# Performance work log

Hardware: AMD Instinct MI355X
Metric: run time of the kernel (lower is better)

Reference implementation:

```python
import jax, jax.numpy as jnp
import numpy as np
import math

N_B = 4
SHAPES = np.array([[100, 100], [50, 50], [25, 25], [13, 13]], dtype=np.int32)
C = 256
M = 8   # heads
L = 4   # levels
P = 4   # points
D = C // M


def _grid_init_bias():
    # matches reset_parameters: per-head directional offsets scaled by point index
    thetas = np.arange(M, dtype=np.float64) * (2.0 * math.pi / M)
    g = np.stack([np.cos(thetas), np.sin(thetas)], -1)
    g = g / np.abs(g).max(-1, keepdims=True)
    g = np.tile(g.reshape(M, 1, 1, 2), (1, L, P, 1))
    g = g * (np.arange(P, dtype=np.float64) + 1.0).reshape(1, 1, P, 1)
    return jnp.asarray(g.reshape(-1), dtype=jnp.float32)


def setup_inputs() -> dict:
    key = jax.random.key(0)
    ks = jax.random.split(key, 10)
    len_in = int((SHAPES[:, 0] * SHAPES[:, 1]).sum())  # 13294
    lq = len_in
    query = jax.random.normal(ks[0], (N_B, lq, C), dtype=jnp.float32)
    reference_points = jax.random.uniform(ks[1], (N_B, lq, L, 2), dtype=jnp.float32)
    input_flatten = jax.random.normal(ks[2], (N_B, len_in, C), dtype=jnp.float32)
    starts = np.concatenate([[0], np.cumsum(SHAPES[:, 0] * SHAPES[:, 1])[:-1]]).astype(np.int32)
    inv_sq = 1.0 / math.sqrt(C)
    Wv = jax.random.normal(ks[3], (C, C), dtype=jnp.float32) * inv_sq
    bv = jnp.zeros((C,), jnp.float32)
    Wo = jax.random.normal(ks[4], (C, C), dtype=jnp.float32) * inv_sq
    bo = jnp.zeros((C,), jnp.float32)
    # torch init zeros these weights; small random values keep the sampling
    # pattern query-dependent (more representative workload)
    W_off = jax.random.normal(ks[5], (C, M * L * P * 2), dtype=jnp.float32) * 1e-3
    b_off = _grid_init_bias()
    W_attn = jax.random.normal(ks[6], (C, M * L * P), dtype=jnp.float32) * 1e-2
    b_attn = jnp.zeros((M * L * P,), jnp.float32)
    return {
        "query": query,
        "reference_points": reference_points,
        "input_flatten": input_flatten,
        "input_space_shape": jnp.asarray(SHAPES),
        "input_level_start_idx": jnp.asarray(starts),
        "Wv": Wv, "bv": bv,
        "W_off": W_off, "b_off": b_off,
        "W_attn": W_attn, "b_attn": b_attn,
        "Wo": Wo, "bo": bo,
    }


def _bilinear_sample(v, lx, ly, H, W):
    """v: (N, M, H*W, D); lx, ly: (N, M, Lq, P) normalized coords in [0,1].
    Equivalent to F.grid_sample(mode='bilinear', padding_mode='zeros',
    align_corners=False) with grid = 2*loc - 1: pixel x = loc*W - 0.5.
    Returns (N, M, Lq, P, D)."""
    n, m, lq, p = lx.shape
    d = v.shape[-1]
    x = lx * W - 0.5
    y = ly * H - 0.5
    x0 = jnp.floor(x)
    y0 = jnp.floor(y)
    wx = x - x0
    wy = y - y0
    x0i = x0.astype(jnp.int32)
    y0i = y0.astype(jnp.int32)
    acc = jnp.zeros((n, m, lq, p, d), dtype=v.dtype)
    corners = [
        (0, 0, (1.0 - wx) * (1.0 - wy)),
        (1, 0, wx * (1.0 - wy)),
        (0, 1, (1.0 - wx) * wy),
        (1, 1, wx * wy),
    ]
    for dx, dy, w in corners:
        xi = x0i + dx
        yi = y0i + dy
        valid = ((xi >= 0) & (xi < W) & (yi >= 0) & (yi < H)).astype(v.dtype)
        idx = jnp.clip(yi, 0, H - 1) * W + jnp.clip(xi, 0, W - 1)  # (N,M,Lq,P)
        g = jnp.take_along_axis(v, idx.reshape(n, m, -1)[..., None], axis=2)
        g = g.reshape(n, m, lq, p, d)
        acc = acc + g * (w * valid)[..., None]
    return acc


def reference(query, reference_points, input_flatten, input_space_shape,
              input_level_start_idx, Wv, bv, W_off, b_off, W_attn, b_attn, Wo, bo):
    n, lq, c = query.shape
    shapes = np.asarray(input_space_shape)  # static (L, 2)
    # value projection -> (N, Len_in, M, D)
    value = (input_flatten @ Wv + bv).reshape(n, -1, M, D)
    # sampling offsets (N, Lq, M, L, P, 2)
    off = (query @ W_off + b_off).reshape(n, lq, M, L, P, 2)
    # attention weights, softmax over L*P
    aw = jax.nn.softmax((query @ W_attn + b_attn).reshape(n, lq, M, L * P), axis=-1)
    aw = aw.reshape(n, lq, M, L, P)
    # normalized sampling locations in [0,1]
    norm = jnp.stack([input_space_shape[:, 1], input_space_shape[:, 0]], -1).astype(query.dtype)  # (L,2) = (W,H)
    loc = reference_points[:, :, None, :, None, :] + off / norm[None, None, None, :, None, :]
    out = jnp.zeros((n, lq, M, D), dtype=query.dtype)
    start = 0
    for lvl in range(shapes.shape[0]):
        H_, W_ = int(shapes[lvl, 0]), int(shapes[lvl, 1])
        v = value[:, start:start + H_ * W_].transpose(0, 2, 1, 3)  # (N, M, HW, D)
        lx = loc[:, :, :, lvl, :, 0].transpose(0, 2, 1, 3)  # (N, M, Lq, P)
        ly = loc[:, :, :, lvl, :, 1].transpose(0, 2, 1, 3)
        s = _bilinear_sample(v, lx, ly, H_, W_)  # (N, M, Lq, P, D)
        out = out + jnp.einsum('nmqpd,nqmp->nqmd', s, aw[:, :, :, lvl])
        start += H_ * W_
    out = out.reshape(n, lq, C)
    return out @ Wo + bo
```

## Files before the change

### kernel.cpp

```cpp
#include <hip/hip_runtime.h>
#include <math.h>

#define NB 4
#define LQ 13294
#define LEN 13294
#define CCH 256
#define MH 8
#define LL 4
#define PP 4
#define DD 32
#define RTOT (NB * LQ)
#define NGRP (RTOT * MH)

typedef short bf16x8 __attribute__((ext_vector_type(8)));
typedef float f32x4  __attribute__((ext_vector_type(4)));

static __device__ __forceinline__ unsigned short f2bf(float f) {
    union { float f; unsigned int u; } v; v.f = f;
    unsigned int r = v.u + 0x7fffu + ((v.u >> 16) & 1u);
    return (unsigned short)(r >> 16);
}

static __device__ __forceinline__ bf16x8 pack8(float4 a, float4 b) {
    bf16x8 r;
    r[0] = (short)f2bf(a.x); r[1] = (short)f2bf(a.y);
    r[2] = (short)f2bf(a.z); r[3] = (short)f2bf(a.w);
    r[4] = (short)f2bf(b.x); r[5] = (short)f2bf(b.y);
    r[6] = (short)f2bf(b.z); r[7] = (short)f2bf(b.w);
    return r;
}

__global__ __launch_bounds__(256) void gemm_mfma_bias(
    const float* __restrict__ A, const float* __restrict__ Bm,
    const float* __restrict__ bias, float* __restrict__ Cm,
    int Rrows, int Nc)
{
    __shared__ unsigned short As[128 * 40];

    const int t    = threadIdx.x;
    const int lane = t & 63;
    const int w    = t >> 6;
    const int wr   = w >> 1;
    const int wc   = w & 1;
    const int blockRow = blockIdx.y * 128;
    const int blockCol = blockIdx.x * 64;

    const int l16 = lane & 15;
    const int kg  = lane >> 4;

    bf16x8 bfr[8][2];
    {
        const float* bp = Bm + (size_t)(kg * 8) * Nc + blockCol + wc * 32 + l16;
#pragma unroll
        for (int ks = 0; ks < 8; ++ks) {
#pragma unroll
            for (int jf = 0; jf < 2; ++jf) {
                bf16x8 bv;
#pragma unroll
                for (int jj = 0; jj < 8; ++jj) {
                    float f = bp[(size_t)(ks * 32 + jj) * Nc + jf * 16];
                    bv[jj] = (short)f2bf(f);
                }
                bfr[ks][jf] = bv;
            }
        }
    }

    const int arow  = t >> 1;
    const int ahalf = t & 1;
    const bool avalid = (blockRow + arow) < Rrows;
    const float* aptr = A + (size_t)(blockRow + arow) * 256 + ahalf * 16;
    unsigned short* wp = &As[arow * 40 + ahalf * 16];

    f32x4 acc[4][2] = {};

    const int arbase = wr * 64 + l16;

#pragma unroll
    for (int ks = 0; ks < 8; ++ks) {
        float4 g0, g1, g2, g3;
        if (avalid) {
            const float* p = aptr + ks * 32;
            g0 = *(const float4*)(p + 0);
            g1 = *(const float4*)(p + 4);
            g2 = *(const float4*)(p + 8);
            g3 = *(const float4*)(p + 12);
        } else {
            g0 = g1 = g2 = g3 = make_float4(0.f, 0.f, 0.f, 0.f);
        }
        __syncthreads();
        *(bf16x8*)(wp + 0) = pack8(g0, g1);
        *(bf16x8*)(wp + 8) = pack8(g2, g3);
        __syncthreads();
#pragma unroll
        for (int i = 0; i < 4; ++i) {
            bf16x8 af = *(const bf16x8*)&As[(arbase + i * 16) * 40 + kg * 8];
            acc[i][0] = __builtin_amdgcn_mfma_f32_16x16x32_bf16(af, bfr[ks][0], acc[i][0], 0, 0, 0);
            acc[i][1] = __builtin_amdgcn_mfma_f32_16x16x32_bf16(af, bfr[ks][1], acc[i][1], 0, 0, 0);
        }
    }

#pragma unroll
    for (int jf = 0; jf < 2; ++jf) {
        const int col = blockCol + wc * 32 + jf * 16 + l16;
        const float bcol = bias[col];
#pragma unroll
        for (int i = 0; i < 4; ++i) {
            const int rbase = blockRow + wr * 64 + i * 16 + kg * 4;
#pragma unroll
            for (int r = 0; r < 4; ++r) {
                const int row = rbase + r;
                if (row < Rrows)
                    Cm[(size_t)row * Nc + col] = acc[i][jf][r] + bcol;
            }
        }
    }
}

__global__ __launch_bounds__(256) void softmax16_kernel(float* __restrict__ aw)
{
    int g = blockIdx.x * 256 + threadIdx.x;
    if (g >= NGRP) return;
    float4* p = (float4*)(aw + (size_t)g * 16);
    float4 v0 = p[0], v1 = p[1], v2 = p[2], v3 = p[3];
    float vals[16] = { v0.x, v0.y, v0.z, v0.w, v1.x, v1.y, v1.z, v1.w,
                       v2.x, v2.y, v2.z, v2.w, v3.x, v3.y, v3.z, v3.w };
    float mx = vals[0];
#pragma unroll
    for (int i = 1; i < 16; ++i) mx = fmaxf(mx, vals[i]);
    float s = 0.f;
#pragma unroll
    for (int i = 0; i < 16; ++i) { vals[i] = expf(vals[i] - mx); s += vals[i]; }
    float inv = 1.f / s;
#pragma unroll
    for (int i = 0; i < 16; ++i) vals[i] *= inv;
    p[0] = make_float4(vals[0], vals[1], vals[2], vals[3]);
    p[1] = make_float4(vals[4], vals[5], vals[6], vals[7]);
    p[2] = make_float4(vals[8], vals[9], vals[10], vals[11]);
    p[3] = make_float4(vals[12], vals[13], vals[14], vals[15]);
}

__global__ __launch_bounds__(256) void sample_kernel(
    const float* __restrict__ value, const float* __restrict__ off,
    const float* __restrict__ aw, const float* __restrict__ refp,
    const int* __restrict__ shapes, const int* __restrict__ starts,
    float* __restrict__ samp)
{
    const int grp = blockIdx.x * 32 + (threadIdx.x >> 3);
    const int l8  = threadIdx.x & 7;
    const int m   = grp & (MH - 1);
    const int row = grp >> 3;
    const int n   = row / LQ;

    const float4 offv = *(const float4*)(off + (size_t)row * 256 + m * 32 + l8 * 4);
    const float2 aw2  = *(const float2*)(aw  + (size_t)row * 128 + m * 16 + l8 * 2);

    const int lvl = l8 >> 1;
    const int H  = shapes[2 * lvl];
    const int W  = shapes[2 * lvl + 1];
    const int st = starts[lvl];
    const float rx = refp[(size_t)row * 8 + lvl * 2 + 0];
    const float ry = refp[(size_t)row * 8 + lvl * 2 + 1];

    int   idx[2][4];
    float wgt[2][4];
#pragma unroll
    for (int s = 0; s < 2; ++s) {
        const float ox = s ? offv.z : offv.x;
        const float oy = s ? offv.w : offv.y;
        const float wa = s ? aw2.y  : aw2.x;
        const float x = fmaf(rx, (float)W, ox) - 0.5f;
        const float y = fmaf(ry, (float)H, oy) - 0.5f;
        const float x0f = floorf(x), y0f = floorf(y);
        const float wx = x - x0f, wy = y - y0f;
        const int x0 = (int)x0f, y0 = (int)y0f;
        const int x1 = x0 + 1,   y1 = y0 + 1;
        const float vx0 = (x0 >= 0 && x0 < W) ? 1.f : 0.f;
        const float vx1 = (x1 >= 0 && x1 < W) ? 1.f : 0.f;
        const float vy0 = (y0 >= 0 && y0 < H) ? 1.f : 0.f;
        const float vy1 = (y1 >= 0 && y1 < H) ? 1.f : 0.f;
        const int xc0 = min(max(x0, 0), W - 1);
        const int xc1 = min(max(x1, 0), W - 1);
        const int rb0 = min(max(y0, 0), H - 1) * W;
        const int rb1 = min(max(y1, 0), H - 1) * W;
        idx[s][0] = st + rb0 + xc0;
        idx[s][1] = st + rb0 + xc1;
        idx[s][2] = st + rb1 + xc0;
        idx[s][3] = st + rb1 + xc1;
        wgt[s][0] = (1.f - wx) * (1.f - wy) * vx0 * vy0 * wa;
        wgt[s][1] = wx * (1.f - wy) * vx1 * vy0 * wa;
        wgt[s][2] = (1.f - wx) * wy * vx0 * vy1 * wa;
        wgt[s][3] = wx * wy * vx1 * vy1 * wa;
    }

    const float* vb = value + (size_t)n * LEN * 256 + m * 32 + l8 * 4;

    float4 acc = make_float4(0.f, 0.f, 0.f, 0.f);
#pragma unroll
    for (int j = 0; j < 16; ++j) {
        const int owner = j >> 1;
        const int s     = j & 1;
#pragma unroll
        for (int c = 0; c < 4; ++c) {
            const int   ic = __shfl(idx[s][c], owner, 8);
            const float wc = __shfl(wgt[s][c], owner, 8);
            const float4 v = *(const float4*)(vb + ((size_t)ic << 8));
            acc.x = fmaf(wc, v.x, acc.x);
            acc.y = fmaf(wc, v.y, acc.y);
            acc.z = fmaf(wc, v.z, acc.z);
            acc.w = fmaf(wc, v.w, acc.w);
        }
    }
    *(float4*)(samp + (size_t)row * 256 + m * 32 + l8 * 4) = acc;
}

extern "C" void kernel_launch(void* const* d_in, const int* in_sizes, int n_in,
                              void* d_out, int out_size, void* d_ws, size_t ws_size,
                              hipStream_t stream)
{
    const float* query  = (const float*)d_in[0];
    const float* refp   = (const float*)d_in[1];
    const float* inp    = (const float*)d_in[2];
    const int*   shapes = (const int*)d_in[3];
    const int*   starts = (const int*)d_in[4];
    const float* Wv     = (const float*)d_in[5];
    const float* bv     = (const float*)d_in[6];
    const float* W_off  = (const float*)d_in[7];
    const float* b_off  = (const float*)d_in[8];
    const float* W_attn = (const float*)d_in[9];
    const float* b_attn = (const float*)d_in[10];
    const float* Wo     = (const float*)d_in[11];
    const float* bo     = (const float*)d_in[12];
    float* out = (float*)d_out;

    float* ws    = (float*)d_ws;
    float* value = ws;
    float* off   = value + (size_t)RTOT * 256;
    float* aw    = off + (size_t)RTOT * 256;
    float* samp  = aw + (size_t)RTOT * 128;

    dim3 blk(256);
    const int rowTiles = (RTOT + 127) / 128;
    dim3 gFull(4, rowTiles);
    dim3 gHalf(2, rowTiles);

    gemm_mfma_bias<<<gFull, blk, 0, stream>>>(inp, Wv, bv, value, RTOT, 256);
    gemm_mfma_bias<<<gFull, blk, 0, stream>>>(query, W_off, b_off, off, RTOT, 256);
    gemm_mfma_bias<<<gHalf, blk, 0, stream>>>(query, W_attn, b_attn, aw, RTOT, 128);
    softmax16_kernel<<<(NGRP + 255) / 256, blk, 0, stream>>>(aw);
    sample_kernel<<<NGRP / 32, blk, 0, stream>>>(value, off, aw, refp, shapes, starts, samp);
    gemm_mfma_bias<<<gFull, blk, 0, stream>>>(samp, Wo, bo, out, RTOT, 256);
}
```

Before: 525.4 us.

## Store intermediates in bf16 and pre-transpose weights for GEMMs

Inputs and query are converted once to bf16 in separate passes, and the weights are transposed and converted to bf16 so each GEMM block loads contiguous 16-byte B fragments instead of doing strided per-element scalar loads. The value projection and the sampled output are now stored in bf16, which halves the gather traffic in the sampling kernel and the A-operand reads of the output GEMM. This costs extra conversion kernel launches and a full read/write pass over query and input, and it lowers the precision of value and of the sampled intermediate.

After: 471.3 us. 10.3% less time.

```diff
diff --git a/kernel.cpp b/kernel.cpp
--- a/kernel.cpp
+++ b/kernel.cpp
@@ -20,7 +20,10 @@
     unsigned int r = v.u + 0x7fffu + ((v.u >> 16) & 1u);
     return (unsigned short)(r >> 16);
 }
-
+static __device__ __forceinline__ float bf2f(unsigned short u) {
+    union { unsigned int u; float f; } v; v.u = ((unsigned int)u) << 16;
+    return v.f;
+}
 static __device__ __forceinline__ bf16x8 pack8(float4 a, float4 b) {
     bf16x8 r;
     r[0] = (short)f2bf(a.x); r[1] = (short)f2bf(a.y);
@@ -30,9 +33,27 @@
     return r;
 }
 
+__global__ __launch_bounds__(256) void cvt_rows_kernel(
+    const float* __restrict__ src, unsigned short* __restrict__ dst)
+{
+    const size_t i = ((size_t)blockIdx.x * 256 + threadIdx.x) * 8;
+    float4 a = *(const float4*)(src + i);
+    float4 b = *(const float4*)(src + i + 4);
+    *(bf16x8*)(dst + i) = pack8(a, b);
+}
+
+__global__ __launch_bounds__(256) void transpose_cvt_kernel(
+    const float* __restrict__ W, unsigned short* __restrict__ Wt, int Nc)
+{
+    const int r = blockIdx.x;
+    const int c = threadIdx.x;
+    if (c < Nc) Wt[(size_t)c * 256 + r] = f2bf(W[(size_t)r * Nc + c]);
+}
+
+template<bool OUT_BF16>
 __global__ __launch_bounds__(256) void gemm_mfma_bias(
-    const float* __restrict__ A, const float* __restrict__ Bm,
-    const float* __restrict__ bias, float* __restrict__ Cm,
+    const unsigned short* __restrict__ A, const unsigned short* __restrict__ Bt,
+    const float* __restrict__ bias, void* __restrict__ Cm,
     int Rrows, int Nc)
 {
     __shared__ unsigned short As[128 * 40];
@@ -50,18 +71,13 @@
 
     bf16x8 bfr[8][2];
     {
-        const float* bp = Bm + (size_t)(kg * 8) * Nc + blockCol + wc * 32 + l16;
+        const unsigned short* bp =
+            Bt + (size_t)(blockCol + wc * 32 + l16) * 256 + kg * 8;
 #pragma unroll
         for (int ks = 0; ks < 8; ++ks) {
 #pragma unroll
             for (int jf = 0; jf < 2; ++jf) {
-                bf16x8 bv;
-#pragma unroll
-                for (int jj = 0; jj < 8; ++jj) {
-                    float f = bp[(size_t)(ks * 32 + jj) * Nc + jf * 16];
-                    bv[jj] = (short)f2bf(f);
-                }
-                bfr[ks][jf] = bv;
+                bfr[ks][jf] = *(const bf16x8*)(bp + (size_t)jf * 16 * 256 + ks * 32);
             }
         }
     }
@@ -69,28 +85,25 @@
     const int arow  = t >> 1;
     const int ahalf = t & 1;
     const bool avalid = (blockRow + arow) < Rrows;
-    const float* aptr = A + (size_t)(blockRow + arow) * 256 + ahalf * 16;
+    const unsigned short* aptr = A + (size_t)(blockRow + arow) * 256 + ahalf * 16;
     unsigned short* wp = &As[arow * 40 + ahalf * 16];
 
     f32x4 acc[4][2] = {};
-
     const int arbase = wr * 64 + l16;
 
 #pragma unroll
     for (int ks = 0; ks < 8; ++ks) {
-        float4 g0, g1, g2, g3;
+        bf16x8 a0, a1;
         if (avalid) {
-            const float* p = aptr + ks * 32;
-            g0 = *(const float4*)(p + 0);
-            g1 = *(const float4*)(p + 4);
-            g2 = *(const float4*)(p + 8);
-            g3 = *(const float4*)(p + 12);
+            const unsigned short* p = aptr + ks * 32;
+            a0 = *(const bf16x8*)(p + 0);
+            a1 = *(const bf16x8*)(p + 8);
         } else {
-            g0 = g1 = g2 = g3 = make_float4(0.f, 0.f, 0.f, 0.f);
+            a0 = (bf16x8)(short)0; a1 = (bf16x8)(short)0;
         }
         __syncthreads();
-        *(bf16x8*)(wp + 0) = pack8(g0, g1);
-        *(bf16x8*)(wp + 8) = pack8(g2, g3);
+        *(bf16x8*)(wp + 0) = a0;
+        *(bf16x8*)(wp + 8) = a1;
         __syncthreads();
 #pragma unroll
         for (int i = 0; i < 4; ++i) {
@@ -110,8 +123,13 @@
 #pragma unroll
             for (int r = 0; r < 4; ++r) {
                 const int row = rbase + r;
-                if (row < Rrows)
-                    Cm[(size_t)row * Nc + col] = acc[i][jf][r] + bcol;
+                if (row < Rrows) {
+                    const float val = acc[i][jf][r] + bcol;
+                    if (OUT_BF16)
+                        ((unsigned short*)Cm)[(size_t)row * Nc + col] = f2bf(val);
+                    else
+                        ((float*)Cm)[(size_t)row * Nc + col] = val;
+                }
             }
         }
     }
@@ -141,10 +159,10 @@
 }
 
 __global__ __launch_bounds__(256) void sample_kernel(
-    const float* __restrict__ value, const float* __restrict__ off,
+    const unsigned short* __restrict__ value, const float* __restrict__ off,
     const float* __restrict__ aw, const float* __restrict__ refp,
     const int* __restrict__ shapes, const int* __restrict__ starts,
-    float* __restrict__ samp)
+    unsigned short* __restrict__ samp)
 {
     const int grp = blockIdx.x * 32 + (threadIdx.x >> 3);
     const int l8  = threadIdx.x & 7;
@@ -193,9 +211,9 @@
         wgt[s][3] = wx * wy * vx1 * vy1 * wa;
     }
 
-    const float* vb = value + (size_t)n * LEN * 256 + m * 32 + l8 * 4;
-
-    float4 acc = make_float4(0.f, 0.f, 0.f, 0.f);
+    const unsigned short* vb = value + (size_t)n * LEN * 256 + m * 32 + l8 * 4;
+
+    float acx = 0.f, acy = 0.f, acz = 0.f, acw = 0.f;
 #pragma unroll
     for (int j = 0; j < 16; ++j) {
         const int owner = j >> 1;
@@ -204,14 +222,16 @@
         for (int c = 0; c < 4; ++c) {
             const int   ic = __shfl(idx[s][c], owner, 8);
             const float wc = __shfl(wgt[s][c], owner, 8);
-            const float4 v = *(const float4*)(vb + ((size_t)ic << 8));
-            acc.x = fmaf(wc, v.x, acc.x);
-            acc.y = fmaf(wc, v.y, acc.y);
-            acc.z = fmaf(wc, v.z, acc.z);
-            acc.w = fmaf(wc, v.w, acc.w);
-        }
-    }
-    *(float4*)(samp + (size_t)row * 256 + m * 32 + l8 * 4) = acc;
+            const ushort4 v = *(const ushort4*)(vb + ((size_t)ic << 8));
+            acx = fmaf(wc, bf2f(v.x), acx);
+            acy = fmaf(wc, bf2f(v.y), acy);
+            acz = fmaf(wc, bf2f(v.z), acz);
+            acw = fmaf(wc, bf2f(v.w), acw);
+        }
+    }
+    ushort4 o;
+    o.x = f2bf(acx); o.y = f2bf(acy); o.z = f2bf(acz); o.w = f2bf(acw);
+    *(ushort4*)(samp + (size_t)row * 256 + m * 32 + l8 * 4) = o;
 }
 
 extern "C" void kernel_launch(void* const* d_in, const int* in_sizes, int n_in,
@@ -233,21 +253,34 @@
     const float* bo     = (const float*)d_in[12];
     float* out = (float*)d_out;
 
-    float* ws    = (float*)d_ws;
-    float* value = ws;
-    float* off   = value + (size_t)RTOT * 256;
-    float* aw    = off + (size_t)RTOT * 256;
-    float* samp  = aw + (size_t)RTOT * 128;
+    float* off = (float*)d_ws;
+    float* aw  = off + (size_t)RTOT * 256;
+    unsigned short* value_bf = (unsigned short*)(aw + (size_t)RTOT * 128);
+    unsigned short* query_bf = value_bf + (size_t)RTOT * 256;
+    unsigned short* inp_bf   = query_bf + (size_t)RTOT * 256;
+    unsigned short* samp_bf  = inp_bf;
+    unsigned short* Wv_t     = inp_bf + (size_t)RTOT * 256;
+    unsigned short* Woff_t   = Wv_t + 256 * 256;
+    unsigned short* Wattn_t  = Woff_t + 256 * 256;
+    unsigned short* Wo_t     = Wattn_t + 128 * 256;
 
     dim3 blk(256);
+    const int cvtBlocks = (int)(((size_t)RTOT * 256) / (256 * 8));
     const int rowTiles = (RTOT + 127) / 128;
     dim3 gFull(4, rowTiles);
     dim3 gHalf(2, rowTiles);
 
-    gemm_mfma_bias<<<gFull, blk, 0, stream>>>(inp, Wv, bv, value, RTOT, 256);
-    gemm_mfma_bias<<<gFull, blk, 0, stream>>>(query, W_off, b_off, off, RTOT, 256);
-    gemm_mfma_bias<<<gHalf, blk, 0, stream>>>(query, W_attn, b_attn, aw, RTOT, 128);
+    cvt_rows_kernel<<<cvtBlocks, blk, 0, stream>>>(inp, inp_bf);
+    cvt_rows_kernel<<<cvtBlocks, blk, 0, stream>>>(query, query_bf);
+    transpose_cvt_kernel<<<256, blk, 0, stream>>>(Wv, Wv_t, 256);
+    transpose_cvt_kernel<<<256, blk, 0, stream>>>(W_off, Woff_t, 256);
+    transpose_cvt_kernel<<<256, blk, 0, stream>>>(W_attn, Wattn_t, 128);
+    transpose_cvt_kernel<<<256, blk, 0, stream>>>(Wo, Wo_t, 256);
+
+    gemm_mfma_bias<true><<<gFull, blk, 0, stream>>>(inp_bf, Wv_t, bv, value_bf, RTOT, 256);
+    gemm_mfma_bias<false><<<gFull, blk, 0, stream>>>(query_bf, Woff_t, b_off, off, RTOT, 256);
+    gemm_mfma_bias<false><<<gHalf, blk, 0, stream>>>(query_bf, Wattn_t, b_attn, aw, RTOT, 128);
     softmax16_kernel<<<(NGRP + 255) / 256, blk, 0, stream>>>(aw);
-    sample_kernel<<<NGRP / 32, blk, 0, stream>>>(value, off, aw, refp, shapes, starts, samp);
-    gemm_mfma_bias<<<gFull, blk, 0, stream>>>(samp, Wo, bo, out, RTOT, 256);
-}
+    sample_kernel<<<NGRP / 32, blk, 0, stream>>>(value_bf, off, aw, refp, shapes, starts, samp_bf);
+    gemm_mfma_bias<false><<<gFull, blk, 0, stream>>>(samp_bf, Wo_t, bo, out, RTOT, 256);
+}
```
